# Kernel tuning notes

Measured on AMD Instinct MI355X. Metric: run time of the kernel, lower is better.

## Reference

```python
import jax, jax.numpy as jnp
import numpy as np

B, N, DIM, H, DH = 4, 2048, 1024, 16, 64

def setup_inputs() -> dict:
    key = jax.random.key(0)
    k1, k2, k3 = jax.random.split(key, 3)
    x = jax.random.normal(k1, (B, N, DIM), dtype=jnp.float32)
    mask = jnp.ones((B, N), dtype=bool)
    w_qkv = jax.random.normal(k2, (DIM, 3 * H * DH), dtype=jnp.float32) * (DIM ** -0.5)
    w_out = jax.random.normal(k3, (H * DH, DIM), dtype=jnp.float32) * ((H * DH) ** -0.5)
    b_out = jnp.zeros((DIM,), dtype=jnp.float32)
    return {"x": x, "mask": mask, "w_qkv": w_qkv, "w_out": w_out, "b_out": b_out}

def reference(x, mask, w_qkv, w_out, b_out):
    b, n, _ = x.shape
    h, dh = H, DH
    scale = dh ** -0.5
    qkv = x @ w_qkv  # [b, n, 3*h*dh]
    q, k, v = jnp.split(qkv, 3, axis=-1)
    # [b, n, h*dh] -> [b, h, n, dh]
    reshape = lambda t: t.reshape(b, n, h, dh).transpose(0, 2, 1, 3)
    q, k, v = reshape(q) * scale, reshape(k), reshape(v)
    dots = jnp.einsum('bhid,bhjd->bhij', q, k)  # materialized N x N scores
    neg = -jnp.finfo(dots.dtype).max
    # key padding mask: [b, j] -> [b, 1, 1, j]
    dots = jnp.where(mask[:, None, None, :], dots, neg)
    # causal mask: mask out j > i
    causal = jnp.triu(jnp.ones((n, n), dtype=bool), k=1)
    dots = jnp.where(causal[None, None, :, :], neg, dots)
    attn = jax.nn.softmax(dots, axis=-1)
    out = jnp.einsum('bhij,bhjd->bhid', attn, v)
    out = out.transpose(0, 2, 1, 3).reshape(b, n, h * dh)
    return out @ w_out + b_out
```

## Files before the change

kernel.cpp:

```cpp
#include <hip/hip_runtime.h>

#define B_   4
#define N_   2048
#define DIM_ 1024
#define H_   16
#define DH_  64
#define NT   (B_ * N_)
#define PS   ((size_t)B_ * H_ * N_ * DH_)

typedef __bf16 bf16x8 __attribute__((ext_vector_type(8)));
typedef short  s16x4  __attribute__((ext_vector_type(4)));
typedef float  f32x4  __attribute__((ext_vector_type(4)));
typedef unsigned int   u32;
typedef unsigned int   u32x2 __attribute__((ext_vector_type(2)));
typedef unsigned short u16;

#define LOG2E 1.44269504088896f
#define QSCALE (0.125f * LOG2E)

__device__ __forceinline__ u16 f2bf(float f) {
  u32 u = __float_as_uint(f);
  u += 0x7FFFu + ((u >> 16) & 1u);
  return (u16)(u >> 16);
}

__device__ __forceinline__ u32 bfpack(float f0, float f1) {
  u32 a = __float_as_uint(f0) + 0x8000u;
  u32 b = __float_as_uint(f1) + 0x8000u;
  return __builtin_amdgcn_perm(b, a, 0x07060302);
}

__device__ __forceinline__ f32x4 mfma32(bf16x8 a, bf16x8 b, f32x4 c) {
  return __builtin_amdgcn_mfma_f32_16x16x32_bf16(a, b, c, 0, 0, 0);
}
__device__ __forceinline__ f32x4 mfma16k(s16x4 a, s16x4 b, f32x4 c) {
  return __builtin_amdgcn_mfma_f32_16x16x16bf16_1k(a, b, c, 0, 0, 0);
}

__device__ __forceinline__ void gld16(const void* g, void* l) {
  __builtin_amdgcn_global_load_lds(
      (const __attribute__((address_space(1))) u32*)g,
      (__attribute__((address_space(3))) u32*)l, 16, 0, 0);
}

__global__ void convert_x_kernel(const float* __restrict__ x, u16* __restrict__ xb) {
  size_t i = ((size_t)blockIdx.x * 256 + threadIdx.x) * 8;
  float4 f0 = *(const float4*)(x + i);
  float4 f1 = *(const float4*)(x + i + 4);
  uint4 o;
  o.x = (u32)f2bf(f0.x) | ((u32)f2bf(f0.y) << 16);
  o.y = (u32)f2bf(f0.z) | ((u32)f2bf(f0.w) << 16);
  o.z = (u32)f2bf(f1.x) | ((u32)f2bf(f1.y) << 16);
  o.w = (u32)f2bf(f1.z) | ((u32)f2bf(f1.w) << 16);
  *(uint4*)(xb + i) = o;
}

__global__ void transpose_conv_kernel(const float* __restrict__ w, u16* __restrict__ wt,
                                      int K, int Ncols) {
  __shared__ u16 T[64 * 66];
  const int n0 = blockIdx.x * 64, k0 = blockIdx.y * 64;
  const int tid = threadIdx.x;
  const int r = tid >> 4, c4 = (tid & 15) * 4;
#pragma unroll
  for (int i = 0; i < 4; ++i) {
    int row = r + i * 16;
    float4 f = *(const float4*)(w + (size_t)(k0 + row) * Ncols + n0 + c4);
    u16* p = &T[row * 66 + c4];
    p[0] = f2bf(f.x); p[1] = f2bf(f.y); p[2] = f2bf(f.z); p[3] = f2bf(f.w);
  }
  __syncthreads();
  const int nr = tid >> 2, kc = (tid & 3) * 16;
  u32 p[8];
#pragma unroll
  for (int j = 0; j < 8; ++j)
    p[j] = (u32)T[(kc + 2 * j) * 66 + nr] | ((u32)T[(kc + 2 * j + 1) * 66 + nr] << 16);
  size_t dst = (size_t)(n0 + nr) * K + k0 + kc;
  *(uint4*)(wt + dst)     = make_uint4(p[0], p[1], p[2], p[3]);
  *(uint4*)(wt + dst + 8) = make_uint4(p[4], p[5], p[6], p[7]);
}

__global__ __launch_bounds__(256) void qkv_gemm_kernel(
    const u16* __restrict__ xb, const u16* __restrict__ wt,
    u16* __restrict__ q, u16* __restrict__ k, u16* __restrict__ vt) {
  __shared__ alignas(16) u16 As[128 * 64];
  __shared__ alignas(16) u16 Bs[128 * 64];
  const int tid = threadIdx.x, wave = tid >> 6, lane = tid & 63;
  const int quad = lane >> 4, l15 = lane & 15;
  const int wm = (wave >> 1) * 64, wn = (wave & 1) * 64;
  const int m0 = blockIdx.y * 128, n0 = blockIdx.x * 128;
  const int srow = lane >> 3;
  const int schunk = (lane & 7) ^ srow;

  f32x4 acc[4][4] = {};

  for (int kt = 0; kt < DIM_; kt += 64) {
    __syncthreads();
#pragma unroll
    for (int i = 0; i < 4; ++i) {
      int c = wave * 4 + i;
      int row = c * 8 + srow;
      gld16(xb + (size_t)(m0 + row) * DIM_ + kt + schunk * 8, As + c * 512);
      gld16(wt + (size_t)(n0 + row) * DIM_ + kt + schunk * 8, Bs + c * 512);
    }
    __syncthreads();
#pragma unroll
    for (int h = 0; h < 2; ++h) {
      bf16x8 af[4], bfr[4];
#pragma unroll
      for (int mi = 0; mi < 4; ++mi) {
        int row = wm + mi * 16 + l15;
        af[mi] = *(const bf16x8*)(As + row * 64 + (((quad + 4 * h) ^ (row & 7)) * 8));
      }
#pragma unroll
      for (int ni = 0; ni < 4; ++ni) {
        int row = wn + ni * 16 + l15;
        bfr[ni] = *(const bf16x8*)(Bs + row * 64 + (((quad + 4 * h) ^ (row & 7)) * 8));
      }
#pragma unroll
      for (int ni = 0; ni < 4; ++ni)
#pragma unroll
        for (int mi = 0; mi < 4; ++mi)
          acc[mi][ni] = mfma32(af[mi], bfr[ni], acc[mi][ni]);
    }
  }

#pragma unroll
  for (int ni = 0; ni < 4; ++ni) {
    int colg = n0 + wn + ni * 16 + l15;
    int part = colg >> 10, rem = colg & 1023;
    int hh = rem >> 6, d = rem & 63;
#pragma unroll
    for (int mi = 0; mi < 4; ++mi) {
      int row0 = m0 + wm + mi * 16 + quad * 4;
      int bb = row0 >> 11, nn0 = row0 & 2047;
      size_t bh = (size_t)(bb * H_ + hh);
      if (part == 0) {
#pragma unroll
        for (int r = 0; r < 4; ++r)
          q[(bh * N_ + nn0 + r) * DH_ + d] = f2bf(acc[mi][ni][r] * QSCALE);
      } else if (part == 1) {
#pragma unroll
        for (int r = 0; r < 4; ++r)
          k[(bh * N_ + nn0 + r) * DH_ + d] = f2bf(acc[mi][ni][r]);
      } else {
        u32 lo = bfpack(acc[mi][ni][0], acc[mi][ni][1]);
        u32 hi = bfpack(acc[mi][ni][2], acc[mi][ni][3]);
        *(uint2*)(vt + (bh * DH_ + d) * N_ + nn0) = make_uint2(lo, hi);
      }
    }
  }
}

__global__ __launch_bounds__(256) void attn_kernel(
    const u16* __restrict__ q, const u16* __restrict__ k,
    const u16* __restrict__ vt, u16* __restrict__ ctx) {
  __shared__ alignas(16) u16 Ks[64 * 64];
  __shared__ alignas(16) u16 Vs[64 * 64];
  const int tid = threadIdx.x, wave = tid >> 6, lane = tid & 63;
  const int quad = lane >> 4, l15 = lane & 15;
  const int p = blockIdx.x;
  const int hh = blockIdx.y, bb = blockIdx.z;
  const int srow = lane >> 3, schunk = (lane & 7) ^ srow;
  const int qtr0 = p, qtr1 = 31 - p;

  const size_t bhofs = (size_t)(bb * H_ + hh) << 17;
  const u16* qp = q + bhofs;
  const u16* kp = k + bhofs;
  const u16* vp = vt + bhofs;

  bf16x8 qf[2][2];
#pragma unroll
  for (int rg = 0; rg < 2; ++rg) {
    int rb = (rg ? qtr1 : qtr0) * 64 + wave * 16 + l15;
#pragma unroll
    for (int h = 0; h < 2; ++h)
      qf[rg][h] = *(const bf16x8*)(qp + (size_t)rb * 64 + h * 32 + quad * 8);
  }

  float m_s[2] = {-INFINITY, -INFINITY};
  float l_s[2] = {0.f, 0.f};
  f32x4 o[2][4] = {};

  const u16* kstage = kp + (size_t)(wave * 16 + srow) * 64 + schunk * 8;
  const u16* vstage = vp + (size_t)(wave * 16 + srow) * N_ + schunk * 8;

  const int jmax = qtr1;
  for (int jt = 0; jt <= jmax; ++jt) {
    __syncthreads();
#pragma unroll
    for (int i = 0; i < 2; ++i) {
      int c = wave * 2 + i;
      gld16(kstage + (size_t)(i * 8) * 64, Ks + c * 512);
      gld16(vstage + (size_t)(i * 8) * N_, Vs + c * 512);
    }
    __syncthreads();
    kstage += 64 * 64;
    vstage += 64;

#pragma unroll
    for (int rg = 0; rg < 2; ++rg) {
      const int qt_rg = rg ? qtr1 : qtr0;
      if (jt > qt_rg) continue;

      f32x4 t[4];
#pragma unroll
      for (int kb = 0; kb < 4; ++kb) {
        int rk = kb * 16 + l15;
        bf16x8 k0 = *(const bf16x8*)(Ks + rk * 64 + ((quad ^ (rk & 7)) * 8));
        bf16x8 k1 = *(const bf16x8*)(Ks + rk * 64 + (((quad + 4) ^ (rk & 7)) * 8));
        f32x4 z = {};
        z = mfma32(k0, qf[rg][0], z);
        z = mfma32(k1, qf[rg][1], z);
        t[kb] = z;
      }
      if (jt == qt_rg) {
        int rloc = wave * 16 + l15;
#pragma unroll
        for (int kb = 0; kb < 4; ++kb)
#pragma unroll
          for (int r = 0; r < 4; ++r)
            if (kb * 16 + quad * 4 + r > rloc) t[kb][r] = -INFINITY;
      }
      float mx = -INFINITY;
#pragma unroll
      for (int kb = 0; kb < 4; ++kb)
#pragma unroll
        for (int r = 0; r < 4; ++r) mx = fmaxf(mx, t[kb][r]);
      mx = fmaxf(mx, __shfl_xor(mx, 16));
      mx = fmaxf(mx, __shfl_xor(mx, 32));
      const float m_old = m_s[rg];
      const float mn = fmaxf(m_old, mx);
      float rs = 0.f;
      u32 pk[8];
#pragma unroll
      for (int kb = 0; kb < 4; ++kb) {
        float p0 = exp2f(t[kb][0] - mn), p1 = exp2f(t[kb][1] - mn);
        float p2 = exp2f(t[kb][2] - mn), p3 = exp2f(t[kb][3] - mn);
        rs += (p0 + p1) + (p2 + p3);
        pk[2 * kb]     = bfpack(p0, p1);
        pk[2 * kb + 1] = bfpack(p2, p3);
      }
      rs += __shfl_xor(rs, 16);
      rs += __shfl_xor(rs, 32);
      if (__any(mx > m_old)) {
        float alpha = exp2f(m_old - mn);
        m_s[rg] = mn;
        l_s[rg] = l_s[rg] * alpha + rs;
#pragma unroll
        for (int db = 0; db < 4; ++db) o[rg][db] *= alpha;
      } else {
        l_s[rg] += rs;
      }

#pragma unroll
      for (int kb = 0; kb < 4; ++kb) {
        u32x2 pp = {pk[2 * kb], pk[2 * kb + 1]};
        s16x4 pbv = __builtin_bit_cast(s16x4, pp);
#pragma unroll
        for (int db = 0; db < 4; ++db) {
          int rv = db * 16 + l15;
          int ch = (2 * kb + (quad >> 1)) ^ (rv & 7);
          s16x4 vf = *(const s16x4*)(Vs + rv * 64 + ch * 8 + (quad & 1) * 4);
          o[rg][db] = mfma16k(vf, pbv, o[rg][db]);
        }
      }
    }
  }

#pragma unroll
  for (int rg = 0; rg < 2; ++rg) {
    float inv = 1.0f / l_s[rg];
    int token = bb * N_ + (rg ? qtr1 : qtr0) * 64 + wave * 16 + l15;
#pragma unroll
    for (int db = 0; db < 4; ++db) {
      u32 lo = bfpack(o[rg][db][0] * inv, o[rg][db][1] * inv);
      u32 hi = bfpack(o[rg][db][2] * inv, o[rg][db][3] * inv);
      *(uint2*)(ctx + (size_t)token * DIM_ + hh * DH_ + db * 16 + quad * 4) =
          make_uint2(lo, hi);
    }
  }
}

__global__ __launch_bounds__(256) void out_gemm_kernel(
    const u16* __restrict__ cb, const u16* __restrict__ wt,
    const float* __restrict__ bias, float* __restrict__ out) {
  __shared__ alignas(16) u16 As[128 * 64];
  __shared__ alignas(16) u16 Bs[128 * 64];
  const int tid = threadIdx.x, wave = tid >> 6, lane = tid & 63;
  const int quad = lane >> 4, l15 = lane & 15;
  const int wm = (wave >> 1) * 64, wn = (wave & 1) * 64;
  const int m0 = blockIdx.y * 128, n0 = blockIdx.x * 128;
  const int srow = lane >> 3;
  const int schunk = (lane & 7) ^ srow;

  f32x4 acc[4][4] = {};

  for (int kt = 0; kt < DIM_; kt += 64) {
    __syncthreads();
#pragma unroll
    for (int i = 0; i < 4; ++i) {
      int c = wave * 4 + i;
      int row = c * 8 + srow;
      gld16(cb + (size_t)(m0 + row) * DIM_ + kt + schunk * 8, As + c * 512);
      gld16(wt + (size_t)(n0 + row) * DIM_ + kt + schunk * 8, Bs + c * 512);
    }
    __syncthreads();
#pragma unroll
    for (int h = 0; h < 2; ++h) {
      bf16x8 af[4], bfr[4];
#pragma unroll
      for (int mi = 0; mi < 4; ++mi) {
        int row = wm + mi * 16 + l15;
        af[mi] = *(const bf16x8*)(As + row * 64 + (((quad + 4 * h) ^ (row & 7)) * 8));
      }
#pragma unroll
      for (int ni = 0; ni < 4; ++ni) {
        int row = wn + ni * 16 + l15;
        bfr[ni] = *(const bf16x8*)(Bs + row * 64 + (((quad + 4 * h) ^ (row & 7)) * 8));
      }
#pragma unroll
      for (int ni = 0; ni < 4; ++ni)
#pragma unroll
        for (int mi = 0; mi < 4; ++mi)
          acc[mi][ni] = mfma32(af[mi], bfr[ni], acc[mi][ni]);
    }
  }

#pragma unroll
  for (int ni = 0; ni < 4; ++ni) {
    int col = n0 + wn + ni * 16 + l15;
    float bv = bias[col];
#pragma unroll
    for (int mi = 0; mi < 4; ++mi) {
      int row0 = m0 + wm + mi * 16 + quad * 4;
#pragma unroll
      for (int r = 0; r < 4; ++r)
        out[(size_t)(row0 + r) * DIM_ + col] = acc[mi][ni][r] + bv;
    }
  }
}

extern "C" void kernel_launch(void* const* d_in, const int* in_sizes, int n_in,
                              void* d_out, int out_size, void* d_ws, size_t ws_size,
                              hipStream_t stream) {
  (void)in_sizes; (void)n_in; (void)out_size; (void)ws_size;
  const float* x     = (const float*)d_in[0];
  const float* w_qkv = (const float*)d_in[2];
  const float* w_out = (const float*)d_in[3];
  const float* b_out = (const float*)d_in[4];
  float* out = (float*)d_out;

  u16* xb_ctx = (u16*)d_ws;
  u16* qw     = xb_ctx + (size_t)NT * DIM_;
  u16* kw     = qw + PS;
  u16* vw     = kw + PS;
  u16* wqkvT  = vw + PS;
  u16* woutT  = wqkvT + (size_t)3072 * 1024;

  convert_x_kernel<<<4096, 256, 0, stream>>>(x, xb_ctx);
  transpose_conv_kernel<<<dim3(48, 16), 256, 0, stream>>>(w_qkv, wqkvT, 1024, 3072);
  transpose_conv_kernel<<<dim3(16, 16), 256, 0, stream>>>(w_out, woutT, 1024, 1024);
  qkv_gemm_kernel<<<dim3(24, 64), 256, 0, stream>>>(xb_ctx, wqkvT, qw, kw, vw);
  attn_kernel<<<dim3(16, 16, 4), 256, 0, stream>>>(qw, kw, vw, xb_ctx);
  out_gemm_kernel<<<dim3(8, 64), 256, 0, stream>>>(xb_ctx, woutT, b_out, out);
}
```

Measured before the change: 293.3 us.

## Widen attention KV tile to 128 keys with per-wave causal skipping

The attention kernel now stages 128 keys of K and V per iteration instead of 64, which halves the number of block-wide barriers and loop iterations. On the diagonal tile, each wave skips MFMA sub-blocks that lie entirely above its causal limit. The softmax rescale is moved ahead of the exp loop so P values feed the PV MFMAs directly without being buffered, and exp2f is replaced with the hardware exp2 intrinsic. The grid is reordered so the batch-head index is the fastest-varying dimension. The trade-offs are twice the LDS footprint, more registers for eight score tiles, and a lower-precision exp.

```diff
diff --git a/kernel.cpp b/kernel.cpp
--- a/kernel.cpp
+++ b/kernel.cpp
@@ -28,6 +28,10 @@
   u32 a = __float_as_uint(f0) + 0x8000u;
   u32 b = __float_as_uint(f1) + 0x8000u;
   return __builtin_amdgcn_perm(b, a, 0x07060302);
+}
+
+__device__ __forceinline__ float fexp2(float x) {
+  return __builtin_amdgcn_exp2f(x);
 }
 
 __device__ __forceinline__ f32x4 mfma32(bf16x8 a, bf16x8 b, f32x4 c) {
@@ -154,13 +158,13 @@
 __global__ __launch_bounds__(256) void attn_kernel(
     const u16* __restrict__ q, const u16* __restrict__ k,
     const u16* __restrict__ vt, u16* __restrict__ ctx) {
-  __shared__ alignas(16) u16 Ks[64 * 64];
-  __shared__ alignas(16) u16 Vs[64 * 64];
+  __shared__ alignas(16) u16 Ks[128 * 64];
+  __shared__ alignas(16) u16 Vs[64 * 128];
   const int tid = threadIdx.x, wave = tid >> 6, lane = tid & 63;
   const int quad = lane >> 4, l15 = lane & 15;
-  const int p = blockIdx.x;
-  const int hh = blockIdx.y, bb = blockIdx.z;
-  const int srow = lane >> 3, schunk = (lane & 7) ^ srow;
+  const int head = blockIdx.x;
+  const int p = blockIdx.y;
+  const int hh = head & 15, bb = head >> 4;
   const int qtr0 = p, qtr1 = 31 - p;
 
   const size_t bhofs = (size_t)(bb * H_ + hh) << 17;
@@ -181,89 +185,92 @@
   float l_s[2] = {0.f, 0.f};
   f32x4 o[2][4] = {};
 
-  const u16* kstage = kp + (size_t)(wave * 16 + srow) * 64 + schunk * 8;
-  const u16* vstage = vp + (size_t)(wave * 16 + srow) * N_ + schunk * 8;
-
-  const int jmax = qtr1;
+  const int ksrow = lane >> 3;
+  const int kschunk = (lane & 7) ^ ksrow;
+  const u16* kstage = kp + (size_t)ksrow * 64 + kschunk * 8;
+  const int vsrow = lane >> 4;
+  const u16* vstage0 = vp + (size_t)vsrow * N_;
+
+  const int jmax = qtr1 >> 1;
   for (int jt = 0; jt <= jmax; ++jt) {
     __syncthreads();
 #pragma unroll
-    for (int i = 0; i < 2; ++i) {
-      int c = wave * 2 + i;
-      gld16(kstage + (size_t)(i * 8) * 64, Ks + c * 512);
-      gld16(vstage + (size_t)(i * 8) * N_, Vs + c * 512);
-    }
-    __syncthreads();
-    kstage += 64 * 64;
-    vstage += 64;
+    for (int i = 0; i < 4; ++i) {
+      int c = wave * 4 + i;
+      gld16(kstage + (size_t)(jt * 128 + c * 8) * 64, Ks + c * 512);
+      int d = c * 4 + vsrow;
+      int vch = (lane & 15) ^ (d & 7);
+      gld16(vstage0 + (size_t)(c * 4) * N_ + jt * 128 + vch * 8, Vs + c * 512);
+    }
+    __syncthreads();
 
 #pragma unroll
     for (int rg = 0; rg < 2; ++rg) {
       const int qt_rg = rg ? qtr1 : qtr0;
-      if (jt > qt_rg) continue;
-
-      f32x4 t[4];
-#pragma unroll
-      for (int kb = 0; kb < 4; ++kb) {
-        int rk = kb * 16 + l15;
-        bf16x8 k0 = *(const bf16x8*)(Ks + rk * 64 + ((quad ^ (rk & 7)) * 8));
-        bf16x8 k1 = *(const bf16x8*)(Ks + rk * 64 + (((quad + 4) ^ (rk & 7)) * 8));
-        f32x4 z = {};
-        z = mfma32(k0, qf[rg][0], z);
-        z = mfma32(k1, qf[rg][1], z);
-        t[kb] = z;
-      }
-      if (jt == qt_rg) {
-        int rloc = wave * 16 + l15;
-#pragma unroll
-        for (int kb = 0; kb < 4; ++kb)
-#pragma unroll
-          for (int r = 0; r < 4; ++r)
-            if (kb * 16 + quad * 4 + r > rloc) t[kb][r] = -INFINITY;
+      if (jt > (qt_rg >> 1)) continue;
+
+      const int rmin = qt_rg * 64 + wave * 16;
+      const int kbmax = min(7, (rmin + 15 - jt * 128) >> 4);
+      const bool diag = (jt == (qt_rg >> 1));
+
+      f32x4 t[8];
+#pragma unroll
+      for (int kb = 0; kb < 8; ++kb) {
+        if (kb <= kbmax) {
+          int rk = kb * 16 + l15;
+          bf16x8 k0 = *(const bf16x8*)(Ks + rk * 64 + ((quad ^ (rk & 7)) * 8));
+          bf16x8 k1 = *(const bf16x8*)(Ks + rk * 64 + (((quad + 4) ^ (rk & 7)) * 8));
+          f32x4 z = {};
+          z = mfma32(k0, qf[rg][0], z);
+          z = mfma32(k1, qf[rg][1], z);
+          if (diag) {
+            int rowl = ((qt_rg & 1) << 6) + wave * 16 + l15;
+#pragma unroll
+            for (int r = 0; r < 4; ++r)
+              if (kb * 16 + quad * 4 + r > rowl) z[r] = -INFINITY;
+          }
+          t[kb] = z;
+        }
       }
       float mx = -INFINITY;
 #pragma unroll
-      for (int kb = 0; kb < 4; ++kb)
-#pragma unroll
-        for (int r = 0; r < 4; ++r) mx = fmaxf(mx, t[kb][r]);
+      for (int kb = 0; kb < 8; ++kb)
+        if (kb <= kbmax)
+#pragma unroll
+          for (int r = 0; r < 4; ++r) mx = fmaxf(mx, t[kb][r]);
       mx = fmaxf(mx, __shfl_xor(mx, 16));
       mx = fmaxf(mx, __shfl_xor(mx, 32));
       const float m_old = m_s[rg];
       const float mn = fmaxf(m_old, mx);
+      if (__any(mx > m_old)) {
+        float alpha = fexp2(m_old - mn);
+        m_s[rg] = mn;
+        l_s[rg] *= alpha;
+#pragma unroll
+        for (int db = 0; db < 4; ++db) o[rg][db] *= alpha;
+      }
       float rs = 0.f;
-      u32 pk[8];
-#pragma unroll
-      for (int kb = 0; kb < 4; ++kb) {
-        float p0 = exp2f(t[kb][0] - mn), p1 = exp2f(t[kb][1] - mn);
-        float p2 = exp2f(t[kb][2] - mn), p3 = exp2f(t[kb][3] - mn);
-        rs += (p0 + p1) + (p2 + p3);
-        pk[2 * kb]     = bfpack(p0, p1);
-        pk[2 * kb + 1] = bfpack(p2, p3);
+#pragma unroll
+      for (int kb = 0; kb < 8; ++kb) {
+        if (kb <= kbmax) {
+          float p0 = fexp2(t[kb][0] - mn), p1 = fexp2(t[kb][1] - mn);
+          float p2 = fexp2(t[kb][2] - mn), p3 = fexp2(t[kb][3] - mn);
+          rs += (p0 + p1) + (p2 + p3);
+          u32x2 pp = {bfpack(p0, p1), bfpack(p2, p3)};
+          s16x4 pbv = __builtin_bit_cast(s16x4, pp);
+          int f = 2 * kb + (quad >> 1);
+#pragma unroll
+          for (int db = 0; db < 4; ++db) {
+            int rv = db * 16 + l15;
+            int ch = f ^ (rv & 7);
+            s16x4 vf = *(const s16x4*)(Vs + rv * 128 + ch * 8 + (quad & 1) * 4);
+            o[rg][db] = mfma16k(vf, pbv, o[rg][db]);
+          }
+        }
       }
       rs += __shfl_xor(rs, 16);
       rs += __shfl_xor(rs, 32);
-      if (__any(mx > m_old)) {
-        float alpha = exp2f(m_old - mn);
-        m_s[rg] = mn;
-        l_s[rg] = l_s[rg] * alpha + rs;
-#pragma unroll
-        for (int db = 0; db < 4; ++db) o[rg][db] *= alpha;
-      } else {
-        l_s[rg] += rs;
-      }
-
-#pragma unroll
-      for (int kb = 0; kb < 4; ++kb) {
-        u32x2 pp = {pk[2 * kb], pk[2 * kb + 1]};
-        s16x4 pbv = __builtin_bit_cast(s16x4, pp);
-#pragma unroll
-        for (int db = 0; db < 4; ++db) {
-          int rv = db * 16 + l15;
-          int ch = (2 * kb + (quad >> 1)) ^ (rv & 7);
-          s16x4 vf = *(const s16x4*)(Vs + rv * 64 + ch * 8 + (quad & 1) * 4);
-          o[rg][db] = mfma16k(vf, pbv, o[rg][db]);
-        }
-      }
+      l_s[rg] += rs;
     }
   }
 
@@ -361,6 +368,6 @@
   transpose_conv_kernel<<<dim3(48, 16), 256, 0, stream>>>(w_qkv, wqkvT, 1024, 3072);
   transpose_conv_kernel<<<dim3(16, 16), 256, 0, stream>>>(w_out, woutT, 1024, 1024);
   qkv_gemm_kernel<<<dim3(24, 64), 256, 0, stream>>>(xb_ctx, wqkvT, qw, kw, vw);
-  attn_kernel<<<dim3(16, 16, 4), 256, 0, stream>>>(qw, kw, vw, xb_ctx);
+  attn_kernel<<<dim3(64, 16), 256, 0, stream>>>(qw, kw, vw, xb_ctx);
   out_gemm_kernel<<<dim3(8, 64), 256, 0, stream>>>(xb_ctx, woutT, b_out, out);
 }
```

Result: faster. 281.5 us (-4.0%).
